# Performance work log

Measured on AMD Instinct MI355X. Metric: run time of the kernel, lower is better.

The kernel has to match this reference:

```python
import jax, jax.numpy as jnp
import numpy as np

B = 8192
K = 64
GLOBAL = 16384  # static size of global index space (fill_max of teacher_indices)
TEMPERATURE = 2.0


def setup_inputs() -> dict:
    key = jax.random.key(0)
    k1, k2, k3 = jax.random.split(key, 3)
    student_logits = jax.random.normal(k1, (B, B), dtype=jnp.float32)
    teacher_scores = jax.random.uniform(k2, (B, K), dtype=jnp.float32)
    batch_indices = jnp.arange(B, dtype=jnp.int32)
    teacher_indices = jax.random.randint(k3, (B, K), 0, GLOBAL, dtype=jnp.int32)
    return {
        "student_logits": student_logits,
        "teacher_scores": teacher_scores,
        "batch_indices": batch_indices,
        "teacher_indices": teacher_indices,
    }


def reference(student_logits, teacher_scores, batch_indices, teacher_indices):
    b = student_logits.shape[0]
    # global -> local mapping table (-1 = not in batch). Static size GLOBAL.
    g2l = jnp.full((GLOBAL,), -1, dtype=jnp.int32).at[batch_indices].set(
        jnp.arange(b, dtype=jnp.int32))
    clamped = jnp.clip(teacher_indices, 0, GLOBAL - 1)
    local_pos = g2l[clamped]                       # [B, K]
    valid = local_pos >= 0
    # invalid entries -> column index b, dropped by scatter mode='drop'
    cols = jnp.where(valid, local_pos, b)
    rows = jnp.broadcast_to(jnp.arange(b, dtype=jnp.int32)[:, None], cols.shape)
    target_probs = jnp.zeros((b, b), dtype=student_logits.dtype)
    target_probs = target_probs.at[rows, cols].set(teacher_scores, mode="drop")
    diag = jnp.arange(b)
    target_probs = target_probs.at[diag, diag].set(1.0)
    row_sums = jnp.clip(target_probs.sum(axis=1, keepdims=True), 1e-8, None)
    target_probs = target_probs / row_sums
    student_log_probs = jax.nn.log_softmax(student_logits / TEMPERATURE, axis=1)
    # KLDivLoss(reduction='batchmean'): sum_t t*(log t - logp) / B, 0 where t==0
    safe_log_t = jnp.log(jnp.where(target_probs > 0, target_probs, 1.0))
    pointwise = jnp.where(target_probs > 0,
                          target_probs * (safe_log_t - student_log_probs), 0.0)
    loss = pointwise.sum() / b
    return loss * (TEMPERATURE ** 2)
```

## Files before the change

### kernel.cpp

```cpp
#include <hip/hip_runtime.h>
#include <math.h>

#define NB 8192
#define NK 64
#define NGLOBAL 16384
#define INV_T 0.5f
#define C_EXP2 0.72134752044448170f


__global__ __launch_bounds__(256) void scatter_kernel(
    const int* __restrict__ bidx, int* __restrict__ g2l, int b) {
    int i = blockIdx.x * blockDim.x + threadIdx.x;
    if (i < b) {
        int g = bidx[i];
        if ((unsigned)g < (unsigned)NGLOBAL) g2l[g] = i;
    }
}

__global__ __launch_bounds__(256) void row_loss_kernel(
    const float* __restrict__ S,
    const float* __restrict__ tscore,
    const int* __restrict__ tindex,
    const int* __restrict__ g2l,
    const int* __restrict__ bidx,
    float* __restrict__ row_out)
{
    const int row = blockIdx.x;
    const int t = threadIdx.x;
    const float* __restrict__ Srow = S + (size_t)row * NB;
    const float4* rp = reinterpret_cast<const float4*>(Srow);

    float4 v[8];
#pragma unroll
    for (int i = 0; i < 8; ++i) v[i] = rp[i * 256 + t];

    int col = -1; bool valid = false; float sc = 0.f, gl = 0.f, gd = 0.f;
    if (t < NK) {
        int gi = tindex[(size_t)row * NK + t];
        gi = min(max(gi, 0), NGLOBAL - 1);
        col = g2l[gi];
        valid = ((unsigned)col < (unsigned)NB) && (bidx[col] == gi)
                && (col != row);
        sc = tscore[(size_t)row * NK + t];
        gl = Srow[valid ? col : row];
        gd = Srow[row];
    }

    asm volatile("" ::: "memory");

    float s0 = 0.f, s1 = 0.f, s2 = 0.f, s3 = 0.f;
#pragma unroll
    for (int i = 0; i < 8; ++i) {
        s0 += exp2f(v[i].x * C_EXP2);
        s1 += exp2f(v[i].y * C_EXP2);
        s2 += exp2f(v[i].z * C_EXP2);
        s3 += exp2f(v[i].w * C_EXP2);
    }
    float s = (s0 + s1) + (s2 + s3);
#pragma unroll
    for (int off = 32; off >= 1; off >>= 1) s += __shfl_xor(s, off);
    __shared__ float sred[4];
    if ((t & 63) == 0) sred[t >> 6] = s;
    __syncthreads();
    const float lse = __logf((sred[0] + sred[1]) + (sred[2] + sred[3]));

    if (t >= NK) return;

    int mycol = valid ? col : -1;
    bool live = valid;
#pragma unroll 1
    for (int k = 1; k < NK; ++k) {
        int ck = __shfl(mycol, k);
        if (valid && t < k && ck == mycol) live = false;
    }

    float part = live ? sc : 0.f;
#pragma unroll
    for (int off = 32; off >= 1; off >>= 1) part += __shfl_xor(part, off);
    const float row_sum = 1.0f + part;

    float term = 0.f;
    if (live && sc > 0.f) {
        float tv = sc / row_sum;
        float logp = fmaf(gl, INV_T, -lse);
        term = tv * (__logf(tv) - logp);
    }
    if (t == 0) {
        float td = 1.0f / row_sum;
        float logp = fmaf(gd, INV_T, -lse);
        term += td * (__logf(td) - logp);
    }
#pragma unroll
    for (int off = 32; off >= 1; off >>= 1) term += __shfl_xor(term, off);
    if (t == 0) row_out[row] = term;
}

__global__ __launch_bounds__(256) void final_reduce_kernel(
    const float* __restrict__ row_out, float* __restrict__ out) {
    const int t = threadIdx.x;
    const float4* rp = reinterpret_cast<const float4*>(row_out);
    float4 w[8];
#pragma unroll
    for (int i = 0; i < 8; ++i) w[i] = rp[i * 256 + t];
    asm volatile("" ::: "memory");
    double acc = 0.0;
#pragma unroll
    for (int i = 0; i < 8; ++i)
        acc += (double)((w[i].x + w[i].y) + (w[i].z + w[i].w));
#pragma unroll
    for (int off = 32; off >= 1; off >>= 1) acc += __shfl_xor(acc, off);
    __shared__ double sd[4];
    if ((t & 63) == 0) sd[t >> 6] = acc;
    __syncthreads();
    if (t == 0) {
        double total = (sd[0] + sd[1]) + (sd[2] + sd[3]);
        out[0] = (float)(total / (double)NB * 4.0);
    }
}

extern "C" void kernel_launch(void* const* d_in, const int* in_sizes, int n_in,
                              void* d_out, int out_size, void* d_ws, size_t ws_size,
                              hipStream_t stream) {
    const float* S      = (const float*)d_in[0];
    const float* tscore = (const float*)d_in[1];
    const int*   bidx   = (const int*)d_in[2];
    const int*   tindex = (const int*)d_in[3];
    float* out = (float*)d_out;
    const int b = in_sizes[2];

    int*   g2l     = (int*)d_ws;
    float* row_out = (float*)((char*)d_ws + NGLOBAL * sizeof(int));

    scatter_kernel<<<(b + 255) / 256, 256, 0, stream>>>(bidx, g2l, b);
    row_loss_kernel<<<NB, 256, 0, stream>>>(S, tscore, tindex, g2l, bidx, row_out);
    final_reduce_kernel<<<1, 256, 0, stream>>>(row_out, out);
}
```

Before: 57.26 us.

## Process two rows per block and use native exp2 builtin

Each block of the row-loss kernel now handles two rows, loading both into registers and running the teacher-index work for each row in its own wavefront. This halves the block count, raises the number of loads in flight per thread and spreads scheduling overhead over twice the work. The exp path switches to the AMDGCN exp2 builtin to avoid the range-checked library exp2f, and the final reduction uses 1024 threads with two loads each. Register pressure doubles for the row data, which may reduce occupancy.

```diff
diff --git a/kernel.cpp b/kernel.cpp
--- a/kernel.cpp
+++ b/kernel.cpp
@@ -6,6 +6,15 @@
 #define NGLOBAL 16384
 #define INV_T 0.5f
 #define C_EXP2 0.72134752044448170f
+
+#if defined(__has_builtin)
+#if __has_builtin(__builtin_amdgcn_exp2f)
+#define EXP2(x) __builtin_amdgcn_exp2f(x)
+#endif
+#endif
+#ifndef EXP2
+#define EXP2(x) exp2f(x)
+#endif
 
 
 __global__ __launch_bounds__(256) void scatter_kernel(
@@ -25,53 +34,73 @@
     const int* __restrict__ bidx,
     float* __restrict__ row_out)
 {
-    const int row = blockIdx.x;
-    const int t = threadIdx.x;
-    const float* __restrict__ Srow = S + (size_t)row * NB;
-    const float4* rp = reinterpret_cast<const float4*>(Srow);
+    const int r0 = blockIdx.x * 2;
+    const int t  = threadIdx.x;
+    const float4* rp0 = reinterpret_cast<const float4*>(S + (size_t)r0 * NB);
+    const float4* rp1 = reinterpret_cast<const float4*>(S + (size_t)(r0 + 1) * NB);
 
-    float4 v[8];
+    float4 v0[8], v1[8];
 #pragma unroll
-    for (int i = 0; i < 8; ++i) v[i] = rp[i * 256 + t];
+    for (int i = 0; i < 8; ++i) v0[i] = rp0[i * 256 + t];
+#pragma unroll
+    for (int i = 0; i < 8; ++i) v1[i] = rp1[i * 256 + t];
 
     int col = -1; bool valid = false; float sc = 0.f, gl = 0.f, gd = 0.f;
-    if (t < NK) {
-        int gi = tindex[(size_t)row * NK + t];
+    const int myrow = r0 + (t >> 6);
+    if (t < 2 * NK) {
+        const int lane = t & 63;
+        const float* __restrict__ Srow = S + (size_t)myrow * NB;
+        int gi = tindex[(size_t)myrow * NK + lane];
         gi = min(max(gi, 0), NGLOBAL - 1);
         col = g2l[gi];
         valid = ((unsigned)col < (unsigned)NB) && (bidx[col] == gi)
-                && (col != row);
-        sc = tscore[(size_t)row * NK + t];
-        gl = Srow[valid ? col : row];
-        gd = Srow[row];
+                && (col != myrow);
+        sc = tscore[(size_t)myrow * NK + lane];
+        gl = Srow[valid ? col : myrow];
+        gd = Srow[myrow];
     }
 
     asm volatile("" ::: "memory");
 
-    float s0 = 0.f, s1 = 0.f, s2 = 0.f, s3 = 0.f;
+    float a0 = 0.f, a1 = 0.f, a2 = 0.f, a3 = 0.f;
+    float b0 = 0.f, b1 = 0.f, b2 = 0.f, b3 = 0.f;
 #pragma unroll
     for (int i = 0; i < 8; ++i) {
-        s0 += exp2f(v[i].x * C_EXP2);
-        s1 += exp2f(v[i].y * C_EXP2);
-        s2 += exp2f(v[i].z * C_EXP2);
-        s3 += exp2f(v[i].w * C_EXP2);
+        a0 += EXP2(v0[i].x * C_EXP2);
+        a1 += EXP2(v0[i].y * C_EXP2);
+        a2 += EXP2(v0[i].z * C_EXP2);
+        a3 += EXP2(v0[i].w * C_EXP2);
     }
-    float s = (s0 + s1) + (s2 + s3);
 #pragma unroll
-    for (int off = 32; off >= 1; off >>= 1) s += __shfl_xor(s, off);
-    __shared__ float sred[4];
-    if ((t & 63) == 0) sred[t >> 6] = s;
+    for (int i = 0; i < 8; ++i) {
+        b0 += EXP2(v1[i].x * C_EXP2);
+        b1 += EXP2(v1[i].y * C_EXP2);
+        b2 += EXP2(v1[i].z * C_EXP2);
+        b3 += EXP2(v1[i].w * C_EXP2);
+    }
+    float sa = (a0 + a1) + (a2 + a3);
+    float sb = (b0 + b1) + (b2 + b3);
+#pragma unroll
+    for (int off = 32; off >= 1; off >>= 1) {
+        sa += __shfl_xor(sa, off);
+        sb += __shfl_xor(sb, off);
+    }
+    __shared__ float sredA[4], sredB[4];
+    if ((t & 63) == 0) { sredA[t >> 6] = sa; sredB[t >> 6] = sb; }
     __syncthreads();
-    const float lse = __logf((sred[0] + sred[1]) + (sred[2] + sred[3]));
+    const float lseA = __logf((sredA[0] + sredA[1]) + (sredA[2] + sredA[3]));
+    const float lseB = __logf((sredB[0] + sredB[1]) + (sredB[2] + sredB[3]));
 
-    if (t >= NK) return;
+    if (t >= 2 * NK) return;
+    const float lse = (t < NK) ? lseA : lseB;
+    const int lane = t & 63;
 
     int mycol = valid ? col : -1;
     bool live = valid;
 #pragma unroll 1
     for (int k = 1; k < NK; ++k) {
         int ck = __shfl(mycol, k);
-        if (valid && t < k && ck == mycol) live = false;
+        if (valid && lane < k && ck == mycol) live = false;
     }
 
     float part = live ? sc : 0.f;
@@ -85,35 +114,33 @@
         float logp = fmaf(gl, INV_T, -lse);
         term = tv * (__logf(tv) - logp);
     }
-    if (t == 0) {
+    if (lane == 0) {
         float td = 1.0f / row_sum;
         float logp = fmaf(gd, INV_T, -lse);
         term += td * (__logf(td) - logp);
     }
 #pragma unroll
     for (int off = 32; off >= 1; off >>= 1) term += __shfl_xor(term, off);
-    if (t == 0) row_out[row] = term;
+    if (lane == 0) row_out[myrow] = term;
 }
 
-__global__ __launch_bounds__(256) void final_reduce_kernel(
+__global__ __launch_bounds__(1024) void final_reduce_kernel(
     const float* __restrict__ row_out, float* __restrict__ out) {
     const int t = threadIdx.x;
     const float4* rp = reinterpret_cast<const float4*>(row_out);
-    float4 w[8];
-#pragma unroll
-    for (int i = 0; i < 8; ++i) w[i] = rp[i * 256 + t];
+    float4 w0 = rp[t], w1 = rp[1024 + t];
     asm volatile("" ::: "memory");
-    double acc = 0.0;
-#pragma unroll
-    for (int i = 0; i < 8; ++i)
-        acc += (double)((w[i].x + w[i].y) + (w[i].z + w[i].w));
+    double acc = (double)((w0.x + w0.y) + (w0.z + w0.w))
+               + (double)((w1.x + w1.y) + (w1.z + w1.w));
 #pragma unroll
     for (int off = 32; off >= 1; off >>= 1) acc += __shfl_xor(acc, off);
-    __shared__ double sd[4];
+    __shared__ double sd[16];
     if ((t & 63) == 0) sd[t >> 6] = acc;
     __syncthreads();
     if (t == 0) {
-        double total = (sd[0] + sd[1]) + (sd[2] + sd[3]);
+        double total = 0.0;
+#pragma unroll
+        for (int i = 0; i < 16; ++i) total += sd[i];
         out[0] = (float)(total / (double)NB * 4.0);
     }
 }
@@ -132,6 +159,6 @@
     float* row_out = (float*)((char*)d_ws + NGLOBAL * sizeof(int));
 
     scatter_kernel<<<(b + 255) / 256, 256, 0, stream>>>(bidx, g2l, b);
-    row_loss_kernel<<<NB, 256, 0, stream>>>(S, tscore, tindex, g2l, bidx, row_out);
-    final_reduce_kernel<<<1, 256, 0, stream>>>(row_out, out);
+    row_loss_kernel<<<NB / 2, 256, 0, stream>>>(S, tscore, tindex, g2l, bidx, row_out);
+    final_reduce_kernel<<<1, 1024, 0, stream>>>(row_out, out);
 }
```

Result: slower. 58.47 us (+2.1%).

## Process four rows per block with register double-buffered prefetch of next row

Applied to the files above, without the earlier changes.

Each block now handles four consecutive rows, loading the next row's data into a second register buffer while computing the current row's log-sum-exp and KL terms. Per-row shared reduction slots avoid a second barrier. It also switches to the raw hardware exp2 builtin and widens the final reduction to 1024 threads. The aim is to hide memory latency and cut per-block launch overhead, at the cost of higher register pressure and fewer blocks.

```diff
diff --git a/kernel.cpp b/kernel.cpp
--- a/kernel.cpp
+++ b/kernel.cpp
@@ -6,6 +6,18 @@
 #define NGLOBAL 16384
 #define INV_T 0.5f
 #define C_EXP2 0.72134752044448170f
+#define RPB 4
+
+#if defined(__has_builtin)
+#if __has_builtin(__builtin_amdgcn_exp2f)
+#define EXP2(x) __builtin_amdgcn_exp2f(x)
+#endif
+#endif
+#ifndef EXP2
+#define EXP2(x) exp2f(x)
+#endif
+
+typedef float f32x4 __attribute__((ext_vector_type(4)));
 
 
 __global__ __launch_bounds__(256) void scatter_kernel(
@@ -17,23 +29,20 @@
     }
 }
 
-__global__ __launch_bounds__(256) void row_loss_kernel(
-    const float* __restrict__ S,
-    const float* __restrict__ tscore,
-    const int* __restrict__ tindex,
-    const int* __restrict__ g2l,
-    const int* __restrict__ bidx,
-    float* __restrict__ row_out)
+__device__ __forceinline__ void process_row(
+    const float* __restrict__ S, const float* __restrict__ tscore,
+    const int* __restrict__ tindex, const int* __restrict__ g2l,
+    const int* __restrict__ bidx, float* __restrict__ row_out,
+    f32x4 (&cur)[8], f32x4 (&nxt)[8], int row, int jbuf, bool prefetch,
+    int t, float (*sred)[4])
 {
-    const int row = blockIdx.x;
-    const int t = threadIdx.x;
+    if (prefetch) {
+        const f32x4* rp = reinterpret_cast<const f32x4*>(S + (size_t)(row + 1) * NB);
+#pragma unroll
+        for (int i = 0; i < 8; ++i) nxt[i] = rp[i * 256 + t];
+    }
+
     const float* __restrict__ Srow = S + (size_t)row * NB;
-    const float4* rp = reinterpret_cast<const float4*>(Srow);
-
-    float4 v[8];
-#pragma unroll
-    for (int i = 0; i < 8; ++i) v[i] = rp[i * 256 + t];
-
     int col = -1; bool valid = false; float sc = 0.f, gl = 0.f, gd = 0.f;
     if (t < NK) {
         int gi = tindex[(size_t)row * NK + t];
@@ -51,69 +60,91 @@
     float s0 = 0.f, s1 = 0.f, s2 = 0.f, s3 = 0.f;
 #pragma unroll
     for (int i = 0; i < 8; ++i) {
-        s0 += exp2f(v[i].x * C_EXP2);
-        s1 += exp2f(v[i].y * C_EXP2);
-        s2 += exp2f(v[i].z * C_EXP2);
-        s3 += exp2f(v[i].w * C_EXP2);
+        s0 += EXP2(cur[i].x * C_EXP2);
+        s1 += EXP2(cur[i].y * C_EXP2);
+        s2 += EXP2(cur[i].z * C_EXP2);
+        s3 += EXP2(cur[i].w * C_EXP2);
     }
     float s = (s0 + s1) + (s2 + s3);
 #pragma unroll
     for (int off = 32; off >= 1; off >>= 1) s += __shfl_xor(s, off);
-    __shared__ float sred[4];
-    if ((t & 63) == 0) sred[t >> 6] = s;
+    if ((t & 63) == 0) sred[jbuf][t >> 6] = s;
     __syncthreads();
-    const float lse = __logf((sred[0] + sred[1]) + (sred[2] + sred[3]));
+    const float lse = __logf((sred[jbuf][0] + sred[jbuf][1]) +
+                             (sred[jbuf][2] + sred[jbuf][3]));
 
-    if (t >= NK) return;
+    if (t < NK) {
+        int mycol = valid ? col : -1;
+        bool live = valid;
+#pragma unroll 1
+        for (int k = 1; k < NK; ++k) {
+            int ck = __shfl(mycol, k);
+            if (valid && t < k && ck == mycol) live = false;
+        }
 
-    int mycol = valid ? col : -1;
-    bool live = valid;
-#pragma unroll 1
-    for (int k = 1; k < NK; ++k) {
-        int ck = __shfl(mycol, k);
-        if (valid && t < k && ck == mycol) live = false;
+        float part = live ? sc : 0.f;
+#pragma unroll
+        for (int off = 32; off >= 1; off >>= 1) part += __shfl_xor(part, off);
+        const float row_sum = 1.0f + part;
+
+        float term = 0.f;
+        if (live && sc > 0.f) {
+            float tv = sc / row_sum;
+            float logp = fmaf(gl, INV_T, -lse);
+            term = tv * (__logf(tv) - logp);
+        }
+        if (t == 0) {
+            float td = 1.0f / row_sum;
+            float logp = fmaf(gd, INV_T, -lse);
+            term += td * (__logf(td) - logp);
+        }
+#pragma unroll
+        for (int off = 32; off >= 1; off >>= 1) term += __shfl_xor(term, off);
+        if (t == 0) row_out[row] = term;
     }
-
-    float part = live ? sc : 0.f;
-#pragma unroll
-    for (int off = 32; off >= 1; off >>= 1) part += __shfl_xor(part, off);
-    const float row_sum = 1.0f + part;
-
-    float term = 0.f;
-    if (live && sc > 0.f) {
-        float tv = sc / row_sum;
-        float logp = fmaf(gl, INV_T, -lse);
-        term = tv * (__logf(tv) - logp);
-    }
-    if (t == 0) {
-        float td = 1.0f / row_sum;
-        float logp = fmaf(gd, INV_T, -lse);
-        term += td * (__logf(td) - logp);
-    }
-#pragma unroll
-    for (int off = 32; off >= 1; off >>= 1) term += __shfl_xor(term, off);
-    if (t == 0) row_out[row] = term;
 }
 
-__global__ __launch_bounds__(256) void final_reduce_kernel(
+__global__ __launch_bounds__(256, 4) void row_loss_kernel(
+    const float* __restrict__ S,
+    const float* __restrict__ tscore,
+    const int* __restrict__ tindex,
+    const int* __restrict__ g2l,
+    const int* __restrict__ bidx,
+    float* __restrict__ row_out)
+{
+    const int r0 = blockIdx.x * RPB;
+    const int t = threadIdx.x;
+    __shared__ float sred[RPB][4];
+
+    f32x4 va[8], vb[8];
+    {
+        const f32x4* rp = reinterpret_cast<const f32x4*>(S + (size_t)r0 * NB);
+#pragma unroll
+        for (int i = 0; i < 8; ++i) va[i] = rp[i * 256 + t];
+    }
+    process_row(S, tscore, tindex, g2l, bidx, row_out, va, vb, r0 + 0, 0, true,  t, sred);
+    process_row(S, tscore, tindex, g2l, bidx, row_out, vb, va, r0 + 1, 1, true,  t, sred);
+    process_row(S, tscore, tindex, g2l, bidx, row_out, va, vb, r0 + 2, 2, true,  t, sred);
+    process_row(S, tscore, tindex, g2l, bidx, row_out, vb, va, r0 + 3, 3, false, t, sred);
+}
+
+__global__ __launch_bounds__(1024) void final_reduce_kernel(
     const float* __restrict__ row_out, float* __restrict__ out) {
     const int t = threadIdx.x;
     const float4* rp = reinterpret_cast<const float4*>(row_out);
-    float4 w[8];
-#pragma unroll
-    for (int i = 0; i < 8; ++i) w[i] = rp[i * 256 + t];
+    float4 w0 = rp[t], w1 = rp[1024 + t];
     asm volatile("" ::: "memory");
-    double acc = 0.0;
-#pragma unroll
-    for (int i = 0; i < 8; ++i)
-        acc += (double)((w[i].x + w[i].y) + (w[i].z + w[i].w));
+    double acc = (double)((w0.x + w0.y) + (w0.z + w0.w))
+               + (double)((w1.x + w1.y) + (w1.z + w1.w));
 #pragma unroll
     for (int off = 32; off >= 1; off >>= 1) acc += __shfl_xor(acc, off);
-    __shared__ double sd[4];
+    __shared__ double sd[16];
     if ((t & 63) == 0) sd[t >> 6] = acc;
     __syncthreads();
     if (t == 0) {
-        double total = (sd[0] + sd[1]) + (sd[2] + sd[3]);
+        double total = 0.0;
+#pragma unroll
+        for (int i = 0; i < 16; ++i) total += sd[i];
         out[0] = (float)(total / (double)NB * 4.0);
     }
 }
@@ -132,6 +163,6 @@
     float* row_out = (float*)((char*)d_ws + NGLOBAL * sizeof(int));
 
     scatter_kernel<<<(b + 255) / 256, 256, 0, stream>>>(bidx, g2l, b);
-    row_loss_kernel<<<NB, 256, 0, stream>>>(S, tscore, tindex, g2l, bidx, row_out);
-    final_reduce_kernel<<<1, 256, 0, stream>>>(row_out, out);
+    row_loss_kernel<<<NB / RPB, 256, 0, stream>>>(S, tscore, tindex, g2l, bidx, row_out);
+    final_reduce_kernel<<<1, 1024, 0, stream>>>(row_out, out);
 }
```

After: 73.93 us. 1.29x slower.
